# Optimization experiments

Hardware: AMD Instinct MI355X
Metric: run time of the kernel (lower is better)

The kernel has to match this reference:

```python
import jax, jax.numpy as jnp
import numpy as np
from jax import lax

B, T = 64, 1000
DEC, ENC, ATT, FILT, KS = 1024, 512, 128, 32, 31
PAD = (KS - 1) // 2


def setup_inputs() -> dict:
    key = jax.random.key(0)
    ks = jax.random.split(key, 9)
    return {
        "decoder_hidden": jax.random.normal(ks[0], (B, DEC), dtype=jnp.float32),
        "encoder_outputs": jax.random.normal(ks[1], (B, T, ENC), dtype=jnp.float32),
        "prev_weights": jax.random.uniform(ks[2], (B, T), dtype=jnp.float32),
        "prev_weights_cum": jax.random.uniform(ks[3], (B, T), dtype=jnp.float32),
        "mask": jnp.zeros((B, T), dtype=bool),
        # learned parameters (torch Linear weight layout: [out, in])
        "conv_w": jax.random.normal(ks[4], (FILT, 2, KS), dtype=jnp.float32) * 0.05,
        "loc_proj_w": jax.random.normal(ks[5], (ATT, FILT), dtype=jnp.float32) * 0.05,
        "query_w": jax.random.normal(ks[6], (ATT, DEC), dtype=jnp.float32) * 0.02,
        "key_w": jax.random.normal(ks[7], (ATT, ENC), dtype=jnp.float32) * 0.02,
        "value_w": jax.random.normal(ks[8], (1, ATT), dtype=jnp.float32) * 0.05,
    }


def reference(decoder_hidden, encoder_outputs, prev_weights, prev_weights_cum,
              mask, conv_w, loc_proj_w, query_w, key_w, value_w):
    # query: (B, ATT)
    query = decoder_hidden @ query_w.T
    # keys: (B, T, ATT)
    keys = jnp.einsum('bte,ae->bta', encoder_outputs, key_w)
    # location features: (B, 2, T) -> conv -> (B, FILT, T)
    loc_feats = jnp.stack([prev_weights, prev_weights_cum], axis=1)
    proc_loc = lax.conv_general_dilated(
        loc_feats, conv_w, window_strides=(1,), padding=[(PAD, PAD)],
        dimension_numbers=('NCH', 'OIH', 'NCH'))
    # (B, T, FILT) -> (B, T, ATT)
    proc_loc = jnp.einsum('bft,af->bta', proc_loc, loc_proj_w)
    # energies: (B, T)
    hidden = jnp.tanh(query[:, None, :] + keys + proc_loc)
    energies = jnp.einsum('bta,a->bt', hidden, value_w[0])
    energies = jnp.where(mask, -jnp.inf, energies)
    attention_weights = jax.nn.softmax(energies, axis=1)
    # context: (B, ENC)
    context = jnp.einsum('bt,bte->be', attention_weights, encoder_outputs)
    return context, attention_weights
```

## Files before the change

kernel.cpp:

```cpp
#include <hip/hip_runtime.h>
#include <hip/hip_bf16.h>
#include <math.h>

#define BB   64
#define TT   1000
#define DEC  1024
#define ENCD 512
#define ATT  128
#define FILT 32
#define KSZ  31
#define PADW 15
#define BT   64
#define KC   64
#define XWN  96

typedef __attribute__((ext_vector_type(8))) short bf16x8;
typedef __attribute__((ext_vector_type(4))) float f32x4;

static __device__ __forceinline__ ushort f2bf(float f) {
    union { float f; unsigned u; } v; v.f = f;
    unsigned r = (v.u + 0x7FFFu + ((v.u >> 16) & 1u)) >> 16;
    return (ushort)r;
}

static __device__ __forceinline__ bf16x8 cvt8(float4 lo, float4 hi) {
    union { __hip_bfloat162 h[4]; bf16x8 v; } u;
    u.h[0] = __float22bfloat162_rn(make_float2(lo.x, lo.y));
    u.h[1] = __float22bfloat162_rn(make_float2(lo.z, lo.w));
    u.h[2] = __float22bfloat162_rn(make_float2(hi.x, hi.y));
    u.h[3] = __float22bfloat162_rn(make_float2(hi.z, hi.w));
    return u.v;
}

static __device__ __forceinline__ float fast_tanh(float x) {
    float e = __expf(2.f * x);
    return 1.f - 2.f * __builtin_amdgcn_rcpf(e + 1.f);
}

static __device__ __forceinline__ void gl2lds16(const void* g, void* l) {
    __builtin_amdgcn_global_load_lds(
        (const __attribute__((address_space(1))) unsigned*)g,
        (__attribute__((address_space(3))) unsigned*)l, 16, 0, 0);
}

__global__ __launch_bounds__(256) void k_prep(const float* __restrict__ kw,
                                              const float* __restrict__ cw,
                                              const float* __restrict__ lpw,
                                              const float* __restrict__ dh,
                                              const float* __restrict__ qw,
                                              const float* __restrict__ vw,
                                              ushort* __restrict__ kwbF,
                                              float* __restrict__ q,
                                              float* __restrict__ Mbuf) {
    __shared__ float qred[128];
    if (blockIdx.x < 32) {
        int idx = blockIdx.x * 256 + threadIdx.x;
        int l  = idx & 63;
        int n  = (idx >> 6) & 7;
        int ks = (idx >> 9) & 1;
        int c  = idx >> 10;
        int a  = n * 16 + (l & 15);
        int k0 = c * 64 + ks * 32 + (l >> 4) * 8;
        ushort u[8];
        #pragma unroll
        for (int j = 0; j < 8; ++j) u[j] = f2bf(kw[a * ENCD + k0 + j]);
        *(uint4*)&kwbF[(size_t)idx * 8] = *(const uint4*)u;
    } else if (blockIdx.x < 36) {
        int idx = (blockIdx.x - 32) * 256 + threadIdx.x;
        int l  = idx & 63;
        int n  = (idx >> 6) & 7;
        int ks = (idx >> 9) & 1;
        int a  = n * 16 + (l & 15);
        int s  = l >> 4;
        ushort u[8];
        #pragma unroll
        for (int j = 0; j < 8; ++j) {
            int k = s * 8 + j;
            float v = 0.f;
            if (k < KSZ) {
                #pragma unroll
                for (int f = 0; f < FILT; ++f)
                    v += cw[(f * 2 + ks) * KSZ + k] * lpw[a * FILT + f];
            }
            u[j] = f2bf(v);
        }
        *(uint4*)&kwbF[(size_t)(((16 + ks) * 8 + n) * 64 + l) * 8] = *(const uint4*)u;
    } else if (blockIdx.x == 36) {
        if (threadIdx.x < 64) {
            float m0 = fabsf(vw[threadIdx.x]) + fabsf(vw[threadIdx.x + 64]);
            #pragma unroll
            for (int off = 1; off < 64; off <<= 1) m0 += __shfl_xor(m0, off, 64);
            if (threadIdx.x == 0) Mbuf[0] = m0;
        }
    } else {
        int b  = blockIdx.x - 37;
        int a  = threadIdx.x & 127;
        int kh = threadIdx.x >> 7;
        const float* dhb = dh + b * DEC + kh * 512;
        const float* qwa = qw + a * DEC + kh * 512;
        float s = 0.f;
        #pragma unroll 4
        for (int k = 0; k < 512; k += 4) {
            float4 x = *(const float4*)&dhb[k];
            float4 w = *(const float4*)&qwa[k];
            s += x.x * w.x + x.y * w.y + x.z * w.z + x.w * w.w;
        }
        if (kh == 1) qred[a] = s;
        __syncthreads();
        if (kh == 0) q[b * ATT + a] = s + qred[a];
    }
}

__global__ __launch_bounds__(256) void k_energies(
    const float* __restrict__ enc, const float* __restrict__ pw,
    const float* __restrict__ pwc, const unsigned char* __restrict__ mask,
    const ushort* __restrict__ kwbF, const float* __restrict__ vw,
    const float* __restrict__ q, const float* __restrict__ Mbuf,
    float* __restrict__ expE, float* __restrict__ pctx,
    float* __restrict__ ps)
{
    __shared__ __align__(16) float Ab[3][BT * 64];
    __shared__ __align__(16) float xw[2][XWN];
    __shared__ float pehalf[2][BT];
    __shared__ float sExp[BT];

    const int b    = blockIdx.x;
    const int tile = blockIdx.y;
    const int t0   = tile * BT;
    const int tid  = threadIdx.x;
    const int w    = tid >> 6;
    const int l    = tid & 63;
    const int r    = l & 15;
    const int sl   = l >> 4;
    const int wt   = w & 1;
    const int wa   = w >> 1;

    const float* encb = enc + (size_t)b * TT * ENCD;

    const int c4src = (l & 15) ^ (w * 4 + (l >> 4));
    const float* aSrc[4];
    #pragma unroll
    for (int j = 0; j < 4; ++j) {
        int rw  = (j * 4 + w) * 4 + (l >> 4);
        int tg  = t0 + rw; if (tg >= TT) tg = TT - 1;
        aSrc[j] = encb + (size_t)tg * ENCD + c4src * 4;
    }

    for (int i = tid; i < 2 * XWN; i += 256) {
        int c  = i / XWN;
        int ii = i - c * XWN;
        int tg = t0 + ii - PADW;
        const float* src = c ? pwc : pw;
        xw[c][ii] = (ii < BT + KSZ - 1 && tg >= 0 && tg < TT) ? src[b * TT + tg] : 0.f;
    }

    uint4 bfr0[2][4], bfr1[2][4];
    auto loadB = [&](uint4 (&dst)[2][4], int c) {
        #pragma unroll
        for (int ks = 0; ks < 2; ++ks)
            #pragma unroll
            for (int nn = 0; nn < 4; ++nn)
                dst[ks][nn] = *(const uint4*)&kwbF[(size_t)(((c * 2 + ks) * 8 + wa * 4 + nn) * 64 + l) * 8];
    };
    auto issueA = [&](int c, int buf) {
        #pragma unroll
        for (int j = 0; j < 4; ++j)
            gl2lds16(aSrc[j] + c * KC, (char*)Ab[buf] + (j * 4 + w) * 1024);
    };

    f32x4 acc[2][4];
    #pragma unroll
    for (int i = 0; i < 2; ++i)
        #pragma unroll
        for (int n = 0; n < 4; ++n) acc[i][n] = (f32x4){0.f, 0.f, 0.f, 0.f};

    auto compute = [&](int c, const uint4 (&bfr)[2][4]) {
        #pragma unroll
        for (int ks = 0; ks < 2; ++ks) {
            const int s2 = 2 * (ks * 4 + sl);
            bf16x8 af[2];
            #pragma unroll
            for (int i = 0; i < 2; ++i) {
                int row = wt * 32 + i * 16 + r;
                if (c < 8) {
                    const char* base = (const char*)Ab[c % 3] + row * 256;
                    float4 alo = *(const float4*)(base + ((s2 ^ r) << 4));
                    float4 ahi = *(const float4*)(base + (((s2 | 1) ^ r) << 4));
                    af[i] = cvt8(alo, ahi);
                } else {
                    const float* xp = &xw[ks][row + sl * 8];
                    float4 alo = make_float4(xp[0], xp[1], xp[2], xp[3]);
                    float4 ahi = make_float4(xp[4], xp[5], xp[6], xp[7]);
                    af[i] = cvt8(alo, ahi);
                }
            }
            __builtin_amdgcn_s_setprio(1);
            #pragma unroll
            for (int i = 0; i < 2; ++i)
                #pragma unroll
                for (int nn = 0; nn < 4; ++nn)
                    acc[i][nn] = __builtin_amdgcn_mfma_f32_16x16x32_bf16(
                        af[i], *(const bf16x8*)&bfr[ks][nn], acc[i][nn], 0, 0, 0);
            __builtin_amdgcn_s_setprio(0);
        }
    };

    issueA(0, 0);
    loadB(bfr0, 0);
    loadB(bfr1, 1);
    issueA(1, 1);
    issueA(2, 2);
    asm volatile("s_waitcnt vmcnt(16) lgkmcnt(0)" ::: "memory");
    __builtin_amdgcn_sched_barrier(0);
    __builtin_amdgcn_s_barrier();

    #pragma unroll
    for (int c = 0; c < 9; ++c) {
        if (c & 1) compute(c, bfr1); else compute(c, bfr0);
        if (c == 8) break;
        __builtin_amdgcn_s_barrier();
        __builtin_amdgcn_sched_barrier(0);
        if (c + 2 <= 8) {
            if (c & 1) loadB(bfr1, c + 2); else loadB(bfr0, c + 2);
        }
        if (c + 3 <= 7) issueA(c + 3, (c + 3) % 3);
        if (c <= 4)      asm volatile("s_waitcnt vmcnt(16)" ::: "memory");
        else if (c == 5) asm volatile("s_waitcnt vmcnt(12)" ::: "memory");
        else if (c == 6) asm volatile("s_waitcnt vmcnt(8)"  ::: "memory");
        else             asm volatile("s_waitcnt vmcnt(0)"  ::: "memory");
        __builtin_amdgcn_sched_barrier(0);
        __builtin_amdgcn_s_barrier();
    }

    const float* qb = q + b * ATT;
    const float M = Mbuf[0];
    float pe[2][4];
    #pragma unroll
    for (int i = 0; i < 2; ++i)
        #pragma unroll
        for (int rr = 0; rr < 4; ++rr) pe[i][rr] = 0.f;
    #pragma unroll
    for (int nn = 0; nn < 4; ++nn) {
        int a = wa * 64 + nn * 16 + r;
        float vvn = vw[a];
        float qvn = qb[a];
        #pragma unroll
        for (int i = 0; i < 2; ++i)
            #pragma unroll
            for (int rr = 0; rr < 4; ++rr)
                pe[i][rr] += vvn * fast_tanh(acc[i][nn][rr] + qvn);
    }
    #pragma unroll
    for (int m = 1; m < 16; m <<= 1)
        #pragma unroll
        for (int i = 0; i < 2; ++i)
            #pragma unroll
            for (int rr = 0; rr < 4; ++rr)
                pe[i][rr] += __shfl_xor(pe[i][rr], m, 64);
    if (r == 0) {
        #pragma unroll
        for (int i = 0; i < 2; ++i)
            #pragma unroll
            for (int rr = 0; rr < 4; ++rr)
                pehalf[wa][wt * 32 + i * 16 + sl * 4 + rr] = pe[i][rr];
    }
    __syncthreads();
    if (tid < BT) {
        int t = t0 + tid;
        float e = pehalf[0][tid] + pehalf[1][tid];
        float v = 0.f;
        if (t < TT && !mask[b * TT + t]) v = __expf(e - M);
        if (t < TT) expE[b * TT + t] = v;
        sExp[tid] = v;
        float sv = v;
        #pragma unroll
        for (int off = 1; off < 64; off <<= 1) sv += __shfl_xor(sv, off, 64);
        if (tid == 0) ps[b * 16 + tile] = sv;
    }
    __syncthreads();

    const int tmax = (TT - t0 < BT) ? (TT - t0) : BT;
    float2 cacc = make_float2(0.f, 0.f);
    const float* pbase = encb + (size_t)t0 * ENCD + tid * 2;
    for (int t = 0; t < tmax; ++t) {
        float s = sExp[t];
        float2 v = *(const float2*)(pbase + (size_t)t * ENCD);
        cacc.x += s * v.x; cacc.y += s * v.y;
    }
    *(float2*)&pctx[(size_t)(b * 16 + tile) * ENCD + tid * 2] = cacc;
}

__global__ __launch_bounds__(256) void k_ctx_reduce(const float* __restrict__ pctx,
                                                    const float* __restrict__ ps,
                                                    const float* __restrict__ expE,
                                                    float* __restrict__ ctx,
                                                    float* __restrict__ wout) {
    int bid = blockIdx.x, tid = threadIdx.x;
    __shared__ float sps[16];
    int b = (bid < BB) ? bid : (bid - BB);
    if (tid < 16) sps[tid] = ps[b * 16 + tid];
    __syncthreads();
    float s = 0.f;
    #pragma unroll
    for (int i = 0; i < 16; ++i) s += sps[i];
    float inv = 1.f / s;
    if (bid < BB) {
        float2 a = make_float2(0.f, 0.f);
        #pragma unroll
        for (int i = 0; i < 16; ++i) {
            float2 v = *(const float2*)&pctx[(size_t)(b * 16 + i) * ENCD + tid * 2];
            a.x += v.x; a.y += v.y;
        }
        a.x *= inv; a.y *= inv;
        *(float2*)&ctx[b * ENCD + tid * 2] = a;
    } else {
        for (int t = tid; t < TT; t += 256)
            wout[b * TT + t] = expE[b * TT + t] * inv;
    }
}

extern "C" void kernel_launch(void* const* d_in, const int* in_sizes, int n_in,
                              void* d_out, int out_size, void* d_ws, size_t ws_size,
                              hipStream_t stream) {
    const float* dh   = (const float*)d_in[0];
    const float* enc  = (const float*)d_in[1];
    const float* pw   = (const float*)d_in[2];
    const float* pwc  = (const float*)d_in[3];
    const unsigned char* mask = (const unsigned char*)d_in[4];
    const float* cw   = (const float*)d_in[5];
    const float* lpw  = (const float*)d_in[6];
    const float* qw   = (const float*)d_in[7];
    const float* kw   = (const float*)d_in[8];
    const float* vw   = (const float*)d_in[9];

    float* out_ctx = (float*)d_out;
    float* out_w   = out_ctx + BB * ENCD;

    float* wsf    = (float*)d_ws;
    float*  q     = wsf;
    float*  expE  = wsf + 8192;
    float*  ps    = wsf + 8192 + 64000;
    float*  pctx  = wsf + 8192 + 64000 + 1024;
    ushort* kwbF  = (ushort*)(wsf + 8192 + 64000 + 1024 + 524288);
    float*  Mbuf  = wsf + 8192 + 64000 + 1024 + 524288 + 36864;

    k_prep    <<<dim3(101),    dim3(256), 0, stream>>>(kw, cw, lpw, dh, qw, vw, kwbF, q, Mbuf);
    k_energies<<<dim3(BB, 16), dim3(256), 0, stream>>>(enc, pw, pwc, mask, kwbF, vw, q, Mbuf, expE, pctx, ps);
    k_ctx_reduce <<<dim3(128), dim3(256), 0, stream>>>(pctx, ps, expE, out_ctx, out_w);
}
```

Baseline: 67.44 us.

## Keep full encoder tile in LDS and reuse it for context accumulation

The LDS A-buffer grows from a 3-deep ring to all 8 K-chunks (about 144KB of float32 LDS per block), so each encoder tile loaded for the key GEMM stays resident. The context partial sum then reads encoder rows from LDS using the swizzled layout instead of re-reading them from global memory. The prefetch pipeline is restructured to run four chunks ahead, with a wait and barrier before each compute step. The larger LDS footprint limits occupancy to one block per CU, which reduces latency hiding.

```diff
diff --git a/kernel.cpp b/kernel.cpp
--- a/kernel.cpp
+++ b/kernel.cpp
@@ -119,7 +119,7 @@
     float* __restrict__ expE, float* __restrict__ pctx,
     float* __restrict__ ps)
 {
-    __shared__ __align__(16) float Ab[3][BT * 64];
+    __shared__ __align__(16) float Ab[9][BT * 64];
     __shared__ __align__(16) float xw[2][XWN];
     __shared__ float pehalf[2][BT];
     __shared__ float sExp[BT];
@@ -162,10 +162,10 @@
             for (int nn = 0; nn < 4; ++nn)
                 dst[ks][nn] = *(const uint4*)&kwbF[(size_t)(((c * 2 + ks) * 8 + wa * 4 + nn) * 64 + l) * 8];
     };
-    auto issueA = [&](int c, int buf) {
+    auto issueA = [&](int c) {
         #pragma unroll
         for (int j = 0; j < 4; ++j)
-            gl2lds16(aSrc[j] + c * KC, (char*)Ab[buf] + (j * 4 + w) * 1024);
+            gl2lds16(aSrc[j] + c * KC, (char*)Ab + c * 16384 + (j * 4 + w) * 1024);
     };
 
     f32x4 acc[2][4];
@@ -183,7 +183,7 @@
             for (int i = 0; i < 2; ++i) {
                 int row = wt * 32 + i * 16 + r;
                 if (c < 8) {
-                    const char* base = (const char*)Ab[c % 3] + row * 256;
+                    const char* base = (const char*)Ab + c * 16384 + row * 256;
                     float4 alo = *(const float4*)(base + ((s2 ^ r) << 4));
                     float4 ahi = *(const float4*)(base + (((s2 | 1) ^ r) << 4));
                     af[i] = cvt8(alo, ahi);
@@ -205,31 +205,29 @@
         }
     };
 
-    issueA(0, 0);
+    issueA(0);
     loadB(bfr0, 0);
+    issueA(1);
     loadB(bfr1, 1);
-    issueA(1, 1);
-    issueA(2, 2);
-    asm volatile("s_waitcnt vmcnt(16) lgkmcnt(0)" ::: "memory");
-    __builtin_amdgcn_sched_barrier(0);
-    __builtin_amdgcn_s_barrier();
+    issueA(2);
+    issueA(3);
 
     #pragma unroll
     for (int c = 0; c < 9; ++c) {
-        if (c & 1) compute(c, bfr1); else compute(c, bfr0);
-        if (c == 8) break;
-        __builtin_amdgcn_s_barrier();
-        __builtin_amdgcn_sched_barrier(0);
-        if (c + 2 <= 8) {
-            if (c & 1) loadB(bfr1, c + 2); else loadB(bfr0, c + 2);
-        }
-        if (c + 3 <= 7) issueA(c + 3, (c + 3) % 3);
-        if (c <= 4)      asm volatile("s_waitcnt vmcnt(16)" ::: "memory");
+        if (c == 0)      asm volatile("s_waitcnt vmcnt(20) lgkmcnt(0)" ::: "memory");
+        else if (c == 1) asm volatile("s_waitcnt vmcnt(20)" ::: "memory");
+        else if (c <= 4) asm volatile("s_waitcnt vmcnt(16)" ::: "memory");
         else if (c == 5) asm volatile("s_waitcnt vmcnt(12)" ::: "memory");
-        else if (c == 6) asm volatile("s_waitcnt vmcnt(8)"  ::: "memory");
+        else if (c <= 7) asm volatile("s_waitcnt vmcnt(8)"  ::: "memory");
         else             asm volatile("s_waitcnt vmcnt(0)"  ::: "memory");
         __builtin_amdgcn_sched_barrier(0);
         __builtin_amdgcn_s_barrier();
+        __builtin_amdgcn_sched_barrier(0);
+        if (c & 1) compute(c, bfr1); else compute(c, bfr0);
+        if (c + 2 <= 8) {
+            if (c & 1) loadB(bfr1, c + 2); else loadB(bfr0, c + 2);
+        }
+        if (c + 4 <= 7) issueA(c + 4);
     }
 
     const float* qb = q + b * ATT;
@@ -279,15 +277,21 @@
     }
     __syncthreads();
 
-    const int tmax = (TT - t0 < BT) ? (TT - t0) : BT;
-    float2 cacc = make_float2(0.f, 0.f);
-    const float* pbase = encb + (size_t)t0 * ENCD + tid * 2;
-    for (int t = 0; t < tmax; ++t) {
-        float s = sExp[t];
-        float2 v = *(const float2*)(pbase + (size_t)t * ENCD);
-        cacc.x += s * v.x; cacc.y += s * v.y;
-    }
-    *(float2*)&pctx[(size_t)(b * 16 + tile) * ENCD + tid * 2] = cacc;
+    {
+        const int col = tid * 2;
+        const int cc  = col >> 6;
+        const int u0  = (col >> 2) & 15;
+        const int sub = (col & 3) * 4;
+        const char* base = (const char*)Ab + cc * 16384 + sub;
+        float2 cacc = make_float2(0.f, 0.f);
+        #pragma unroll 4
+        for (int t = 0; t < BT; ++t) {
+            float s = sExp[t];
+            float2 v = *(const float2*)(base + t * 256 + (((u0 ^ (t & 15))) << 4));
+            cacc.x += s * v.x; cacc.y += s * v.y;
+        }
+        *(float2*)&pctx[(size_t)(b * 16 + tile) * ENCD + col] = cacc;
+    }
 }
 
 __global__ __launch_bounds__(256) void k_ctx_reduce(const float* __restrict__ pctx,
```

New measurement: 70.39 us. +4.4%, slower.
